# Optimization experiments

Hardware: AMD Instinct MI355X
Metric: run time of the kernel (lower is better)

## Reference

```python
import jax, jax.numpy as jnp
import numpy as np

B, N, C = 8192, 4, 768          # B = batch*tokens, N = n_streams, C = dim
HID = 4 * C                      # FFN hidden
EPS_RMS = 1.1920929e-7           # torch.finfo(float32).eps (nn.RMSNorm default eps=None)
EPS_SK = 1e-6                    # sinkhorn eps
SK_ITERS = 20
ALPHA = 0.01


def setup_inputs() -> dict:
    key = jax.random.key(0)
    ks = jax.random.split(key, 7)
    w = lambda k, shape: (jax.random.normal(k, shape, jnp.float32) * 0.02)
    return {
        "x": jax.random.normal(ks[0], (B, N, C), jnp.float32),
        "norm_w": jnp.ones((N * C,), jnp.float32),
        "w_pre": w(ks[1], (N, N * C)),
        "b_pre": jnp.zeros((N,), jnp.float32),
        "w_post": w(ks[2], (N, N * C)),
        "b_post": jnp.zeros((N,), jnp.float32),
        "w_res": w(ks[3], (N * N, N * C)),
        "b_res": jnp.zeros((N * N,), jnp.float32),
        "alpha_pre": jnp.array(ALPHA, jnp.float32),
        "alpha_post": jnp.array(ALPHA, jnp.float32),
        "alpha_res": jnp.array(ALPHA, jnp.float32),
        "w1": w(ks[4], (HID, C)),   # torch Linear weight layout [out, in]
        "b1": jnp.zeros((HID,), jnp.float32),
        "w2": w(ks[5], (C, HID)),
        "b2": jnp.zeros((C,), jnp.float32),
    }


def sinkhorn_knopp(logits):
    # logits: [B, n, n] -> doubly-stochastic matrix via 20 row/col normalizations
    M0 = jnp.exp(logits)

    def body(_, M):
        M = M / (M.sum(axis=-1, keepdims=True) + EPS_SK)
        M = M / (M.sum(axis=-2, keepdims=True) + EPS_SK)
        return M

    return jax.lax.fori_loop(0, SK_ITERS, body, M0)


def reference(x, norm_w, w_pre, b_pre, w_post, b_post, w_res, b_res,
              alpha_pre, alpha_post, alpha_res, w1, b1, w2, b2):
    b, n, c = x.shape
    x_flat = x.reshape(b, n * c)
    # RMSNorm over flattened streams
    x_norm = x_flat * jax.lax.rsqrt(jnp.mean(x_flat * x_flat, axis=-1, keepdims=True) + EPS_RMS) * norm_w
    # gate logits
    pre = alpha_pre * (x_norm @ w_pre.T) + b_pre            # [B, n]
    post = alpha_post * (x_norm @ w_post.T) + b_post        # [B, n]
    res_logits = (alpha_res * (x_norm @ w_res.T) + b_res).reshape(b, n, n)
    H_pre = jax.nn.sigmoid(pre)
    H_post = 2.0 * jax.nn.sigmoid(post)
    H_res = sinkhorn_knopp(res_logits)                      # [B, n, n]
    # pre-gate + stream mixing
    x_pre = x * H_pre[..., None]                            # [B, n, C]
    x_streams = jnp.einsum('bij,bjc->bic', H_res, x_pre)
    # fn = FFN applied on [B*n, C]
    h = jax.nn.gelu(x_streams.reshape(b * n, c) @ w1.T + b1, approximate=False)
    y = (h @ w2.T + b2).reshape(b, n, c)
    y = y * H_post[..., None]
    # residual mixed by the same DSM
    res = jnp.einsum('bij,bjc->bic', H_res, x)
    return res + y
```

## Files before the change

kernel.cpp:

```cpp
#include <hip/hip_runtime.h>

#define EPS_RMS 1.1920929e-7f
#define EPS_SK  1e-6f

typedef __bf16 bf16;
typedef __bf16 bf16x4 __attribute__((ext_vector_type(4)));
typedef __bf16 bf16x8 __attribute__((ext_vector_type(8)));
typedef float  f32x4  __attribute__((ext_vector_type(4)));

typedef __attribute__((address_space(3))) void lds_void;
typedef __attribute__((address_space(1))) void glb_void;

__device__ __forceinline__ void async_copy16(void* lds_dst, const void* gsrc) {
  __builtin_amdgcn_global_load_lds((glb_void*)gsrc, (lds_void*)lds_dst, 16, 0, 0);
}

template<int N> __device__ __forceinline__ void wait_vmcnt() {
  if constexpr (N == 6)      asm volatile("s_waitcnt vmcnt(6)" ::: "memory");
  else if constexpr (N == 5) asm volatile("s_waitcnt vmcnt(5)" ::: "memory");
  else                       asm volatile("s_waitcnt vmcnt(0)" ::: "memory");
}
__device__ __forceinline__ void lgkm0_fence() {
  asm volatile("s_waitcnt lgkmcnt(0)" ::: "memory");
  __builtin_amdgcn_sched_barrier(0);
}

__device__ __forceinline__ void xcd_swizzle(int& bx, int& by) {
  const int gx = gridDim.x, nwg = gx * gridDim.y;
  const int flat = blockIdx.y * gx + blockIdx.x;
  const int q = nwg >> 3, r = nwg & 7;
  const int xcd = flat & 7, i = flat >> 3;
  const int lin = (xcd < r ? xcd * (q + 1) : r * (q + 1) + (xcd - r) * q) + i;
  bx = lin % gx;
  by = lin / gx;
}

__global__ __launch_bounds__(256) void convert_w_kernel(
    const float* __restrict__ w1, const float* __restrict__ w2,
    bf16* __restrict__ w1b, bf16* __restrict__ w2b) {
  size_t i = ((size_t)blockIdx.x * 256 + threadIdx.x) * 4;
  f32x4 a = *(const f32x4*)(w1 + i);
  f32x4 b = *(const f32x4*)(w2 + i);
  bf16x4 ab, bb;
#pragma unroll
  for (int q = 0; q < 4; ++q) { ab[q] = (bf16)a[q]; bb[q] = (bf16)b[q]; }
  *(bf16x4*)(w1b + i) = ab;
  *(bf16x4*)(w2b + i) = bb;
}

__global__ __launch_bounds__(256) void prep_wnb_kernel(
    const float* __restrict__ w_pre, const float* __restrict__ w_post,
    const float* __restrict__ w_res, const float* __restrict__ norm_w,
    bf16* __restrict__ wnb) {
  const int i = (blockIdx.x * 256 + threadIdx.x) * 4;
  const int j = i / 3072, k = i - j * 3072;
  f32x4 wv;
  if (j < 24) {
    const float* src = j < 4 ? (w_pre + j * 3072)
                     : (j < 8 ? (w_post + (j - 4) * 3072) : (w_res + (j - 8) * 3072));
    const f32x4 nv = *(const f32x4*)(norm_w + k);
    wv = *(const f32x4*)(src + k);
    wv = wv * nv;
  } else {
    wv = f32x4{0.f, 0.f, 0.f, 0.f};
  }
  bf16x4 o;
#pragma unroll
  for (int q = 0; q < 4; ++q) o[q] = (bf16)wv[q];
  *(bf16x4*)(wnb + i) = o;
}

__global__ __launch_bounds__(256) void gates_kernel(
    const float* __restrict__ x, const bf16* __restrict__ wnb,
    const float* __restrict__ b_pre, const float* __restrict__ b_post,
    const float* __restrict__ b_res,
    const float* __restrict__ alpha_pre, const float* __restrict__ alpha_post,
    const float* __restrict__ alpha_res, float* __restrict__ gates,
    bf16* __restrict__ xs, bf16* __restrict__ resb) {
  const int t = threadIdx.x, wv = t >> 6, l = t & 63;
  const int r0 = blockIdx.x * 16;
  __shared__ float buf[4][16][32];
  __shared__ float bsq[4][16];
  __shared__ float gm[16][20];

  f32x4 acc[2] = {};
  float sq = 0.f;
  const int kbase = wv * 768;
  const size_t arow = (size_t)(r0 + (l & 15)) * 3072;
  const int koff = (l >> 4) * 8;
#pragma unroll 1
  for (int ks = 0; ks < 24; ++ks) {
    const int k0 = kbase + ks * 32 + koff;
    const f32x4 a0 = *(const f32x4*)(x + arow + k0);
    const f32x4 a1 = *(const f32x4*)(x + arow + k0 + 4);
    sq += a0[0]*a0[0] + a0[1]*a0[1] + a0[2]*a0[2] + a0[3]*a0[3]
        + a1[0]*a1[0] + a1[1]*a1[1] + a1[2]*a1[2] + a1[3]*a1[3];
    bf16x8 af;
#pragma unroll
    for (int e = 0; e < 4; ++e) { af[e] = (bf16)a0[e]; af[4 + e] = (bf16)a1[e]; }
#pragma unroll
    for (int nf = 0; nf < 2; ++nf) {
      const bf16x8 bn = *(const bf16x8*)(wnb + (size_t)(nf * 16 + (l & 15)) * 3072 + k0);
      acc[nf] = __builtin_amdgcn_mfma_f32_16x16x32_bf16(af, bn, acc[nf], 0, 0, 0);
    }
  }
  sq += __shfl_xor(sq, 16);
  sq += __shfl_xor(sq, 32);
#pragma unroll
  for (int nf = 0; nf < 2; ++nf)
#pragma unroll
    for (int j = 0; j < 4; ++j)
      buf[wv][(l >> 4) * 4 + j][nf * 16 + (l & 15)] = acc[nf][j];
  if (l < 16) bsq[wv][l] = sq;
  __syncthreads();

  if (t < 16) {
    const int r = t;
    float dv[24];
#pragma unroll
    for (int j = 0; j < 24; ++j)
      dv[j] = buf[0][r][j] + buf[1][r][j] + buf[2][r][j] + buf[3][r][j];
    const float ssq = bsq[0][r] + bsq[1][r] + bsq[2][r] + bsq[3][r];
    const float rms = rsqrtf(ssq * (1.f / 3072.f) + EPS_RMS);
    const float ap = alpha_pre[0], apo = alpha_post[0], ar = alpha_res[0];
    float* g = gates + (size_t)(r0 + r) * 24;
    float M[16];
    float hp[4];
#pragma unroll
    for (int j = 0; j < 4; ++j) {
      const float p = ap * rms * dv[j] + b_pre[j];
      hp[j] = 1.f / (1.f + __expf(-p));
      g[j] = hp[j];
      const float q = apo * rms * dv[4 + j] + b_post[j];
      g[4 + j] = 2.f / (1.f + __expf(-q));
    }
#pragma unroll
    for (int j = 0; j < 16; ++j) M[j] = __expf(ar * rms * dv[8 + j] + b_res[j]);
    for (int it = 0; it < 20; ++it) {
#pragma unroll
      for (int i = 0; i < 4; ++i) {
        const float s = M[i * 4] + M[i * 4 + 1] + M[i * 4 + 2] + M[i * 4 + 3] + EPS_SK;
        const float ri = __fdividef(1.f, s);
#pragma unroll
        for (int j = 0; j < 4; ++j) M[i * 4 + j] *= ri;
      }
#pragma unroll
      for (int j = 0; j < 4; ++j) {
        const float s = M[j] + M[4 + j] + M[8 + j] + M[12 + j] + EPS_SK;
        const float ri = __fdividef(1.f, s);
#pragma unroll
        for (int i = 0; i < 4; ++i) M[i * 4 + j] *= ri;
      }
    }
#pragma unroll
    for (int j = 0; j < 16; ++j) { g[8 + j] = M[j]; gm[r][j] = M[j]; }
#pragma unroll
    for (int j = 0; j < 4; ++j) gm[r][16 + j] = hp[j];
  }
  __syncthreads();

  const int bb = t >> 4, tt = t & 15;
  float mr[4][4], mp[4][4];
#pragma unroll
  for (int i = 0; i < 4; ++i)
#pragma unroll
    for (int j = 0; j < 4; ++j) {
      mr[i][j] = gm[bb][i * 4 + j];
      mp[i][j] = mr[i][j] * gm[bb][16 + j];
    }
  const size_t xb = (size_t)(r0 + bb) * 3072;
#pragma unroll 1
  for (int cc = 0; cc < 12; ++cc) {
    const int c4 = (tt + cc * 16) * 4;
    f32x4 xj[4];
#pragma unroll
    for (int j = 0; j < 4; ++j)
      xj[j] = *(const f32x4*)(x + xb + (size_t)j * 768 + c4);
#pragma unroll
    for (int i = 0; i < 4; ++i) {
      f32x4 vr = mr[i][0] * xj[0] + mr[i][1] * xj[1] + mr[i][2] * xj[2] + mr[i][3] * xj[3];
      f32x4 vs = mp[i][0] * xj[0] + mp[i][1] * xj[1] + mp[i][2] * xj[2] + mp[i][3] * xj[3];
      bf16x4 ro, so;
#pragma unroll
      for (int q = 0; q < 4; ++q) { ro[q] = (bf16)vr[q]; so[q] = (bf16)vs[q]; }
      *(bf16x4*)(resb + xb + (size_t)i * 768 + c4) = ro;
      *(bf16x4*)(xs   + xb + (size_t)i * 768 + c4) = so;
    }
  }
}

__device__ __forceinline__ void stage_block(
    const bf16* __restrict__ src, const int rowBase, const int K, const int k0,
    char* ldsBuf, const int blk, const int t) {
  const int r = t >> 3;
  const int c = (t & 7) ^ (r & 7);
  async_copy16(ldsBuf + blk * 8192 + t * 16,
               src + (size_t)(rowBase + blk * 64 + r) * K + k0 + c * 8);
}

template<int NB>
__device__ __forceinline__ void gemm256_core(
    const bf16* __restrict__ A, const bf16* __restrict__ B, const int K,
    const int tM, const int tN, char* AL, char* BL, f32x4 (&acc)[8][NB]) {
  constexpr int BBUF = NB * 8192;
  const int t = threadIdx.x, l = t & 63, w = t >> 6;
  const int wr = w >> 2, wc = w & 3;
  const int NT = K >> 6;
  const int arow = wr * 128 + (l & 15);
  const int brow = wc * (NB * 16) + (l & 15);
  const int cb = l >> 4;

  auto frag = [&](const char* base, int row, int ks) -> bf16x8 {
    const int c = ks * 4 + cb;
    return *(const bf16x8*)(base + row * 128 + ((c ^ (row & 7)) << 4));
  };

#pragma unroll
  for (int b = 0; b < 4; ++b) stage_block(A, tM, K, 0, AL, b, t);
#pragma unroll
  for (int b = 0; b < NB; ++b) stage_block(B, tN, K, 0, BL, b, t);
  stage_block(A, tM, K, 64, AL + 32768, 0, t);
  stage_block(A, tM, K, 64, AL + 32768, 2, t);
#pragma unroll
  for (int b = 0; b < NB; ++b) stage_block(B, tN, K, 64, BL + BBUF, b, t);
  wait_vmcnt<NB + 2>();
  __builtin_amdgcn_s_barrier();

  for (int T = 0; T < NT; ++T) {
    char* Ab = AL + (T & 1) * 32768;
    char* Bb = BL + (T & 1) * BBUF;
    char* An = AL + ((T + 1) & 1) * 32768;
    const int k1 = (T + 1) << 6, k2 = (T + 2) << 6;
    const bool s1 = (T + 1 < NT), s2 = (T + 2 < NT);
    bf16x8 af[4][2], bfv[NB][2];

#pragma unroll
    for (int ks = 0; ks < 2; ++ks) {
#pragma unroll
      for (int ni = 0; ni < NB; ++ni) bfv[ni][ks] = frag(Bb, brow + ni * 16, ks);
#pragma unroll
      for (int mi = 0; mi < 4; ++mi) af[mi][ks] = frag(Ab, arow + mi * 16, ks);
    }
    __builtin_amdgcn_s_barrier();
    if (s1) { stage_block(A, tM, K, k1, An, 1, t); stage_block(A, tM, K, k1, An, 3, t); }
    lgkm0_fence();
    __builtin_amdgcn_s_setprio(1);
#pragma unroll
    for (int ks = 0; ks < 2; ++ks)
#pragma unroll
      for (int mi = 0; mi < 4; ++mi)
#pragma unroll
        for (int ni = 0; ni < NB; ++ni)
          acc[mi][ni] = __builtin_amdgcn_mfma_f32_16x16x32_bf16(af[mi][ks], bfv[ni][ks], acc[mi][ni], 0, 0, 0);
    __builtin_amdgcn_s_setprio(0);

#pragma unroll
    for (int ks = 0; ks < 2; ++ks)
#pragma unroll
      for (int mi = 0; mi < 4; ++mi) af[mi][ks] = frag(Ab, arow + (4 + mi) * 16, ks);
    __builtin_amdgcn_s_barrier();
    if (s2) {
      stage_block(A, tM, K, k2, Ab, 0, t); stage_block(A, tM, K, k2, Ab, 2, t);
#pragma unroll
      for (int b = 0; b < NB; ++b) stage_block(B, tN, K, k2, Bb, b, t);
    }
    if (T < NT - 2)       wait_vmcnt<NB + 2>();
    else if (T == NT - 2) wait_vmcnt<0>();
    lgkm0_fence();
    __builtin_amdgcn_s_setprio(1);
#pragma unroll
    for (int ks = 0; ks < 2; ++ks)
#pragma unroll
      for (int mi = 0; mi < 4; ++mi)
#pragma unroll
        for (int ni = 0; ni < NB; ++ni)
          acc[4 + mi][ni] = __builtin_amdgcn_mfma_f32_16x16x32_bf16(af[mi][ks], bfv[ni][ks], acc[4 + mi][ni], 0, 0, 0);
    __builtin_amdgcn_s_setprio(0);
  }
}

__global__ __launch_bounds__(512, 1) void ffn1_kernel(
    const bf16* __restrict__ xs, const bf16* __restrict__ w1b,
    const float* __restrict__ b1, bf16* __restrict__ h) {
  __shared__ __align__(16) char AL[2 * 32768];
  __shared__ __align__(16) char BL[2 * 32768];
  int bx, by; xcd_swizzle(bx, by);
  const int tM = by * 256, tN = bx * 256;
  f32x4 acc[8][4] = {};
  gemm256_core<4>(xs, w1b, 768, tM, tN, AL, BL, acc);

  const int t = threadIdx.x, l = t & 63;
  const int w = t >> 6, wr = w >> 2, wc = w & 3;
  float bias[4];
#pragma unroll
  for (int ni = 0; ni < 4; ++ni) bias[ni] = b1[tN + wc * 64 + ni * 16 + (l & 15)];
#pragma unroll
  for (int mi = 0; mi < 8; ++mi)
#pragma unroll
    for (int j = 0; j < 4; ++j) {
      const int m = tM + wr * 128 + mi * 16 + (l >> 4) * 4 + j;
#pragma unroll
      for (int ni = 0; ni < 4; ++ni) {
        const int n = tN + wc * 64 + ni * 16 + (l & 15);
        const float v = acc[mi][ni][j] + bias[ni];
        const float y2 = 1.5957691216f * (v + 0.044715f * v * v * v);
        const float g = __fdividef(v, 1.f + __expf(-y2));
        h[(size_t)m * 3072 + n] = (bf16)g;
      }
    }
}

__global__ __launch_bounds__(512, 1) void ffn2_kernel(
    const bf16* __restrict__ h, const bf16* __restrict__ w2b,
    const float* __restrict__ b2, const float* __restrict__ gates,
    const bf16* __restrict__ resb, float* __restrict__ outp, const int m0) {
  __shared__ __align__(16) char AL[2 * 32768];
  __shared__ __align__(16) char BL[2 * 24576];
  int bx, by; xcd_swizzle(bx, by);
  const int tM = by * 256, tN = bx * 192;
  f32x4 acc[8][3] = {};
  gemm256_core<3>(h, w2b, 3072, tM, tN, AL, BL, acc);

  const int t = threadIdx.x, l = t & 63;
  const int w = t >> 6, wr = w >> 2, wc = w & 3;
  float bias[3];
#pragma unroll
  for (int ni = 0; ni < 3; ++ni) bias[ni] = b2[tN + wc * 48 + ni * 16 + (l & 15)];
#pragma unroll
  for (int mi = 0; mi < 8; ++mi)
#pragma unroll
    for (int j = 0; j < 4; ++j) {
      const int mL = tM + wr * 128 + mi * 16 + (l >> 4) * 4 + j;
      const int mG = m0 + mL;
      const float hp = gates[(size_t)(mG >> 2) * 24 + 4 + (mG & 3)];
#pragma unroll
      for (int ni = 0; ni < 3; ++ni) {
        const int n = tN + wc * 48 + ni * 16 + (l & 15);
        const size_t o = (size_t)mG * 768 + n;
        outp[o] = (float)resb[o] + (acc[mi][ni][j] + bias[ni]) * hp;
      }
    }
}

extern "C" void kernel_launch(void* const* d_in, const int* in_sizes, int n_in,
                              void* d_out, int out_size, void* d_ws, size_t ws_size,
                              hipStream_t stream) {
  (void)in_sizes; (void)n_in; (void)out_size;
  const float* x         = (const float*)d_in[0];
  const float* norm_w    = (const float*)d_in[1];
  const float* w_pre     = (const float*)d_in[2];
  const float* b_pre     = (const float*)d_in[3];
  const float* w_post    = (const float*)d_in[4];
  const float* b_post    = (const float*)d_in[5];
  const float* w_res     = (const float*)d_in[6];
  const float* b_res     = (const float*)d_in[7];
  const float* alpha_pre = (const float*)d_in[8];
  const float* alpha_post= (const float*)d_in[9];
  const float* alpha_res = (const float*)d_in[10];
  const float* w1        = (const float*)d_in[11];
  const float* b1        = (const float*)d_in[12];
  const float* w2        = (const float*)d_in[13];
  const float* b2        = (const float*)d_in[14];
  float* outp = (float*)d_out;

  char* ws = (char*)d_ws;
  float* gates = (float*)ws;
  bf16*  w1b   = (bf16*)(ws + 786432);
  bf16*  w2b   = (bf16*)(ws + 5505024);
  bf16*  xs    = (bf16*)(ws + 10223616);
  bf16*  resb  = (bf16*)(ws + 60555264);
  bf16*  wnb   = (bf16*)(ws + 110886912);
  bf16*  h     = (bf16*)(ws + 111083520);

  size_t avail = ws_size > 111083520 ? ws_size - 111083520 : 0;
  long hrows = (long)(avail / (3072 * 2));
  hrows = (hrows / 256) * 256;
  if (hrows > 32768) hrows = 32768;
  if (hrows < 256) hrows = 256;

  convert_w_kernel<<<dim3(2304), dim3(256), 0, stream>>>(w1, w2, w1b, w2b);
  prep_wnb_kernel<<<dim3(96), dim3(256), 0, stream>>>(w_pre, w_post, w_res, norm_w, wnb);
  gates_kernel<<<dim3(512), dim3(256), 0, stream>>>(
      x, wnb, b_pre, b_post, b_res, alpha_pre, alpha_post, alpha_res, gates, xs, resb);

  for (long mo = 0; mo < 32768; mo += hrows) {
    const long mm = (32768 - mo) < hrows ? (32768 - mo) : hrows;
    ffn1_kernel<<<dim3(12, (unsigned)(mm / 256)), dim3(512), 0, stream>>>(
        xs + mo * 768, w1b, b1, h);
    ffn2_kernel<<<dim3(4, (unsigned)(mm / 256)), dim3(512), 0, stream>>>(
        h, w2b, b2, gates, resb, outp, (int)mo);
  }
}
```

Before: 482.0 us.

## Stage GEMM epilogues through LDS for vectorized stores and simplify A prefetch

The FFN1 and FFN2 epilogues now write accumulator tiles to a per-wave LDS scratch area and then read them back row-contiguously. This lets h be stored as 16-byte bf16x8 vectors, and the residual load plus output store become f32x4/bf16x4 vectors, replacing scattered 2- or 4-byte accesses. The GEMM core also drops the split A prefetch, which loaded half of the next tile early, and instead loads all four A blocks two tiles ahead, with vmcnt waits adjusted to match. This adds LDS round trips and a __syncthreads, and reduces the finer-grained overlap of A loads.

```diff
diff --git a/kernel.cpp b/kernel.cpp
--- a/kernel.cpp
+++ b/kernel.cpp
@@ -16,7 +16,9 @@
 }
 
 template<int N> __device__ __forceinline__ void wait_vmcnt() {
-  if constexpr (N == 6)      asm volatile("s_waitcnt vmcnt(6)" ::: "memory");
+  if constexpr (N == 8)      asm volatile("s_waitcnt vmcnt(8)" ::: "memory");
+  else if constexpr (N == 7) asm volatile("s_waitcnt vmcnt(7)" ::: "memory");
+  else if constexpr (N == 6) asm volatile("s_waitcnt vmcnt(6)" ::: "memory");
   else if constexpr (N == 5) asm volatile("s_waitcnt vmcnt(5)" ::: "memory");
   else                       asm volatile("s_waitcnt vmcnt(0)" ::: "memory");
 }
@@ -219,19 +221,18 @@
   for (int b = 0; b < 4; ++b) stage_block(A, tM, K, 0, AL, b, t);
 #pragma unroll
   for (int b = 0; b < NB; ++b) stage_block(B, tN, K, 0, BL, b, t);
-  stage_block(A, tM, K, 64, AL + 32768, 0, t);
-  stage_block(A, tM, K, 64, AL + 32768, 2, t);
+#pragma unroll
+  for (int b = 0; b < 4; ++b) stage_block(A, tM, K, 64, AL + 32768, b, t);
 #pragma unroll
   for (int b = 0; b < NB; ++b) stage_block(B, tN, K, 64, BL + BBUF, b, t);
-  wait_vmcnt<NB + 2>();
+  wait_vmcnt<NB + 4>();
   __builtin_amdgcn_s_barrier();
 
   for (int T = 0; T < NT; ++T) {
     char* Ab = AL + (T & 1) * 32768;
     char* Bb = BL + (T & 1) * BBUF;
-    char* An = AL + ((T + 1) & 1) * 32768;
-    const int k1 = (T + 1) << 6, k2 = (T + 2) << 6;
-    const bool s1 = (T + 1 < NT), s2 = (T + 2 < NT);
+    const int k2 = (T + 2) << 6;
+    const bool s2 = (T + 2 < NT);
     bf16x8 af[4][2], bfv[NB][2];
 
 #pragma unroll
@@ -242,7 +243,6 @@
       for (int mi = 0; mi < 4; ++mi) af[mi][ks] = frag(Ab, arow + mi * 16, ks);
     }
     __builtin_amdgcn_s_barrier();
-    if (s1) { stage_block(A, tM, K, k1, An, 1, t); stage_block(A, tM, K, k1, An, 3, t); }
     lgkm0_fence();
     __builtin_amdgcn_s_setprio(1);
 #pragma unroll
@@ -260,11 +260,12 @@
       for (int mi = 0; mi < 4; ++mi) af[mi][ks] = frag(Ab, arow + (4 + mi) * 16, ks);
     __builtin_amdgcn_s_barrier();
     if (s2) {
-      stage_block(A, tM, K, k2, Ab, 0, t); stage_block(A, tM, K, k2, Ab, 2, t);
+#pragma unroll
+      for (int b = 0; b < 4; ++b) stage_block(A, tM, K, k2, Ab, b, t);
 #pragma unroll
       for (int b = 0; b < NB; ++b) stage_block(B, tN, K, k2, Bb, b, t);
     }
-    if (T < NT - 2)       wait_vmcnt<NB + 2>();
+    if (T < NT - 2)       wait_vmcnt<NB + 4>();
     else if (T == NT - 2) wait_vmcnt<0>();
     lgkm0_fence();
     __builtin_amdgcn_s_setprio(1);
@@ -294,20 +295,33 @@
   float bias[4];
 #pragma unroll
   for (int ni = 0; ni < 4; ++ni) bias[ni] = b1[tN + wc * 64 + ni * 16 + (l & 15)];
-#pragma unroll
-  for (int mi = 0; mi < 8; ++mi)
+
+  __syncthreads();
+  float* wlds = (float*)(AL + w * 8192);
+#pragma unroll 1
+  for (int mi = 0; mi < 8; ++mi) {
 #pragma unroll
     for (int j = 0; j < 4; ++j) {
-      const int m = tM + wr * 128 + mi * 16 + (l >> 4) * 4 + j;
+      const int r = (l >> 4) * 4 + j;
 #pragma unroll
       for (int ni = 0; ni < 4; ++ni) {
-        const int n = tN + wc * 64 + ni * 16 + (l & 15);
         const float v = acc[mi][ni][j] + bias[ni];
         const float y2 = 1.5957691216f * (v + 0.044715f * v * v * v);
-        const float g = __fdividef(v, 1.f + __expf(-y2));
-        h[(size_t)m * 3072 + n] = (bf16)g;
+        wlds[r * 68 + ni * 16 + (l & 15)] = __fdividef(v, 1.f + __expf(-y2));
       }
     }
+    const int rr = l >> 3, c0 = (l & 7) * 8;
+#pragma unroll
+    for (int half = 0; half < 2; ++half) {
+      const int row = rr + half * 8;
+      const f32x4 u0 = *(const f32x4*)(wlds + row * 68 + c0);
+      const f32x4 u1 = *(const f32x4*)(wlds + row * 68 + c0 + 4);
+      bf16x8 ov;
+#pragma unroll
+      for (int q = 0; q < 4; ++q) { ov[q] = (bf16)u0[q]; ov[4 + q] = (bf16)u1[q]; }
+      *(bf16x8*)(h + (size_t)(tM + wr * 128 + mi * 16 + row) * 3072 + tN + wc * 64 + c0) = ov;
+    }
+  }
 }
 
 __global__ __launch_bounds__(512, 1) void ffn2_kernel(
@@ -326,20 +340,33 @@
   float bias[3];
 #pragma unroll
   for (int ni = 0; ni < 3; ++ni) bias[ni] = b2[tN + wc * 48 + ni * 16 + (l & 15)];
-#pragma unroll
-  for (int mi = 0; mi < 8; ++mi)
+
+  __syncthreads();
+  float* wlds = (float*)(AL + w * 8192);
+#pragma unroll 1
+  for (int mi = 0; mi < 8; ++mi) {
 #pragma unroll
     for (int j = 0; j < 4; ++j) {
-      const int mL = tM + wr * 128 + mi * 16 + (l >> 4) * 4 + j;
-      const int mG = m0 + mL;
+      const int r = (l >> 4) * 4 + j;
+#pragma unroll
+      for (int ni = 0; ni < 3; ++ni)
+        wlds[r * 52 + ni * 16 + (l & 15)] = acc[mi][ni][j] + bias[ni];
+    }
+#pragma unroll
+    for (int rep = 0; rep < 3; ++rep) {
+      const int unit = rep * 64 + l;
+      const int row = unit / 12;
+      const int cs = unit - row * 12;
+      const int mG = m0 + tM + wr * 128 + mi * 16 + row;
       const float hp = gates[(size_t)(mG >> 2) * 24 + 4 + (mG & 3)];
-#pragma unroll
-      for (int ni = 0; ni < 3; ++ni) {
-        const int n = tN + wc * 48 + ni * 16 + (l & 15);
-        const size_t o = (size_t)mG * 768 + n;
-        outp[o] = (float)resb[o] + (acc[mi][ni][j] + bias[ni]) * hp;
-      }
-    }
+      const f32x4 v = *(const f32x4*)(wlds + row * 52 + cs * 4);
+      const bf16x4 rb = *(const bf16x4*)(resb + (size_t)mG * 768 + tN + wc * 48 + cs * 4);
+      f32x4 o;
+#pragma unroll
+      for (int q = 0; q < 4; ++q) o[q] = (float)rb[q] + v[q] * hp;
+      *(f32x4*)(outp + (size_t)mG * 768 + tN + wc * 48 + cs * 4) = o;
+    }
+  }
 }
 
 extern "C" void kernel_launch(void* const* d_in, const int* in_sizes, int n_in,
```

Result: slower. 822.6 us (+70.7%).
